# Performance work log

Measured on AMD Instinct MI355X. Metric: run time of the kernel, lower is better.

The kernel has to match this reference:

```python
import jax, jax.numpy as jnp
import numpy as np

IN_F, OUT_F = 2048, 2048
IQ, OQ = IN_F // 4, OUT_F // 4
B, S = 4, 4096


def _xavier(key, shape):
    fan_out, fan_in = shape
    limit = float(np.sqrt(6.0 / (fan_in + fan_out)))
    return jax.random.uniform(key, shape, jnp.float32, -limit, limit)


def setup_inputs() -> dict:
    key = jax.random.key(0)
    kx, kr, ki, kj, kk = jax.random.split(key, 5)
    return {
        "x": jax.random.normal(kx, (B, S, IN_F), dtype=jnp.float32),
        "wr": _xavier(kr, (OQ, IQ)),
        "wi": _xavier(ki, (OQ, IQ)),
        "wj": _xavier(kj, (OQ, IQ)),
        "wk": _xavier(kk, (OQ, IQ)),
        "bias": jnp.zeros((OUT_F,), dtype=jnp.float32),
    }


def reference(x, wr, wi, wj, wk, bias):
    b, s, _ = x.shape
    iq = wr.shape[1]
    oq = wr.shape[0]
    # strided quaternion component extraction: x[..., c::4] -> (B*S, iq)
    xq = x.reshape(b * s, iq, 4)  # last-dim interleaved layout
    xr, xi, xj, xk = xq[..., 0], xq[..., 1], xq[..., 2], xq[..., 3]
    # small GEMMs against W^T (W is (oq, iq)); only the products actually used
    Ar = xr @ wr.T
    Br = xi @ wr.T
    Cr = xj @ wr.T
    Dr = xk @ wr.T
    Ai = xr @ wi.T
    Bi = xi @ wi.T
    Aj = xr @ wj.T
    Cj = xj @ wj.T
    Ak = xr @ wk.T
    Dk = xk @ wk.T
    # combine exactly as in the original module
    or_ = Ar - Bi - Cj - Dk
    oi_ = Br + Ai + Dk - Cj
    oj_ = Cr - Dk + Aj + Bi
    ok_ = Dr + Cj - Bi + Ak
    # interleaved scatter: out[:, c::4] = o<c>
    out = jnp.stack([or_, oi_, oj_, ok_], axis=-1).reshape(b, s, 4 * oq)
    return out + bias[None, None, :]
```

## Files before the change

kernel.cpp:

```cpp
#include <hip/hip_runtime.h>


typedef unsigned short u16;
typedef __bf16 bf16x8 __attribute__((ext_vector_type(8)));
typedef float f32x16 __attribute__((ext_vector_type(16)));

#define QM 16384
#define QN 2048
#define QK 2048

__device__ __forceinline__ u16 f2bf(float f) {
    union { float f; unsigned u; } v;
    v.f = f;
    unsigned r = v.u + 0x7FFFu + ((v.u >> 16) & 1u);
    return (u16)(r >> 16);
}

__device__ __forceinline__ void async_copy16(const u16* g, u16* l) {
    __builtin_amdgcn_global_load_lds(
        (const __attribute__((address_space(1))) void*)g,
        (__attribute__((address_space(3))) void*)l,
        16, 0, 0);
}

__global__ void prep_kernel(const float* __restrict__ x, u16* __restrict__ xb,
                            const float* __restrict__ wr, const float* __restrict__ wi,
                            const float* __restrict__ wj, const float* __restrict__ wk,
                            u16* __restrict__ wb) {
    const int b = blockIdx.x;
    if (b < 4096) {
        const int n4 = (QM * QK) / 4;
        for (int i = b * blockDim.x + threadIdx.x; i < n4; i += 4096 * blockDim.x) {
            float4 v = reinterpret_cast<const float4*>(x)[i];
            ushort4 o;
            o.x = f2bf(v.x); o.y = f2bf(v.y); o.z = f2bf(v.z); o.w = f2bf(v.w);
            reinterpret_cast<ushort4*>(xb)[i] = o;
        }
    } else {
        int i = (b - 4096) * blockDim.x + threadIdx.x;
        int n = i >> 9;
        int p = i & 511;
        int q = n >> 2, co = n & 3;
        int base = (q << 9) + p;
        float r  = wr[base], ii = wi[base], jj = wj[base], kk = wk[base];
        float e0, e1, e2, e3;
        if      (co == 0) { e0 = r;  e1 = -ii; e2 = -jj; e3 = -kk; }
        else if (co == 1) { e0 = ii; e1 = r;   e2 = -jj; e3 = kk;  }
        else if (co == 2) { e0 = jj; e1 = ii;  e2 = r;   e3 = -kk; }
        else              { e0 = kk; e1 = -ii; e2 = jj;  e3 = r;   }
        ushort4 o;
        o.x = f2bf(e0); o.y = f2bf(e1); o.z = f2bf(e2); o.w = f2bf(e3);
        reinterpret_cast<ushort4*>(wb)[(n << 9) + p] = o;
    }
}

__global__ __launch_bounds__(512, 2) void qgemm_kernel(const u16* __restrict__ A,
                                                       const u16* __restrict__ B,
                                                       const float* __restrict__ bias,
                                                       float* __restrict__ C) {
    __shared__ __align__(16) u16 L[81920];

    const int bid = blockIdx.x;
    const int swz = (bid & 7) * 64 + (bid >> 3);
    const int bm = swz >> 3;
    const int bn = swz & 7;

    const int tid = threadIdx.x;
    const int wid = tid >> 6, lane = tid & 63;
    const int wm = wid >> 2, wn = wid & 3;
    const int lr = lane & 31;
    const int hi = lane >> 5;
    
    const u16* Asrc = A + (size_t)bm * 256 * QK;
    const u16* Bsrc = B + (size_t)bn * 256 * QK;

    const int rA  = tid >> 3;
    const int clA = ((tid & 7) ^ (rA & 7)) << 3;
    const size_t soff = (size_t)rA * QK + clA;

    f32x16 acc[4][2];
#pragma unroll
    for (int i = 0; i < 4; ++i)
#pragma unroll
        for (int j = 0; j < 2; ++j)
            acc[i][j] = (f32x16){0.f};

    auto stage = [&](const u16* src, int lbase, int k0) {
#pragma unroll
        for (int o = 0; o < 2; ++o)
            async_copy16(src + (size_t)(o * 64) * QK + k0 + soff,
                         &L[lbase + o * 4096 + wid * 512]);
    };

    auto rdA = [&](const u16* LA, int mt, int s) -> bf16x8 {
        const int r = wm * 128 + mt * 32 + lr;
        const int c = ((s * 2 + hi) ^ (r & 7)) << 3;
        return *(const bf16x8*)&LA[r * 64 + c];
    };
    auto rdB = [&](const u16* LB, int nt, int s) -> bf16x8 {
        const int r = wn * 64 + nt * 32 + lr;
        const int c = ((s * 2 + hi) ^ (r & 7)) << 3;
        return *(const bf16x8*)&LB[r * 64 + c];
    };

    auto doTile = [&](const int ab, const int bt, const int bt2, const int t)
        __attribute__((always_inline)) {
        const u16* LA = &L[ab * 16384];
        const u16* LB = &L[32768 + bt * 16384];
        const int tw1 = (t + 1) & 31, tw2 = (t + 2) & 31;
        const int oA = (ab ^ 1) * 16384;
        const int oB = 32768 + bt2 * 16384;

#pragma unroll
        for (int s = 0; s < 4; ++s) {
            bf16x8 bv[2], av[4];
#pragma unroll
            for (int nt = 0; nt < 2; ++nt) bv[nt] = rdB(LB, nt, s);
#pragma unroll
            for (int mt = 0; mt < 4; ++mt) av[mt] = rdA(LA, mt, s);
            if      (s == 0) stage(Asrc,            oA,        tw1 * 64);
            else if (s == 1) stage(Asrc + 128 * QK, oA + 8192, tw1 * 64);
            else if (s == 2) stage(Bsrc,            oB,        tw2 * 64);
            else             stage(Bsrc + 128 * QK, oB + 8192, tw2 * 64);
#pragma unroll
            for (int mt = 0; mt < 4; ++mt)
#pragma unroll
                for (int nt = 0; nt < 2; ++nt)
                    acc[mt][nt] = __builtin_amdgcn_mfma_f32_32x32x16_bf16(
                        av[mt], bv[nt], acc[mt][nt], 0, 0, 0);
        }

        asm volatile("s_waitcnt lgkmcnt(0) vmcnt(4)" ::: "memory");
        __builtin_amdgcn_s_barrier();
    };

    stage(Asrc,            0,             0);
    stage(Asrc + 128 * QK, 8192,          0);
    stage(Bsrc,            32768,             0);
    stage(Bsrc + 128 * QK, 32768 + 8192,      0);
    stage(Bsrc,            32768 + 16384,        64);
    stage(Bsrc + 128 * QK, 32768 + 16384 + 8192, 64);
    asm volatile("s_waitcnt vmcnt(4)" ::: "memory");
    __builtin_amdgcn_s_barrier();

    for (int t = 0; t < 30; t += 6) {
        doTile(0, 0, 2, t);
        doTile(1, 1, 0, t + 1);
        doTile(0, 2, 1, t + 2);
        doTile(1, 0, 2, t + 3);
        doTile(0, 1, 0, t + 4);
        doTile(1, 2, 1, t + 5);
    }
    doTile(0, 0, 2, 30);
    doTile(1, 1, 0, 31);

    const int colbase = bn * 256 + wn * 64;
    const int rowbase = bm * 256 + wm * 128;
    float bsv[2];
#pragma unroll
    for (int nt = 0; nt < 2; ++nt) bsv[nt] = bias[colbase + nt * 32 + lr];
    float* Cb = C + (size_t)rowbase * QN + colbase;
#pragma unroll
    for (int mt = 0; mt < 4; ++mt)
#pragma unroll
        for (int nt = 0; nt < 2; ++nt)
#pragma unroll
            for (int e = 0; e < 16; ++e) {
                const int ro = mt * 32 + (e & 3) + 8 * (e >> 2) + 4 * hi;
                Cb[(size_t)ro * QN + nt * 32 + lr] = acc[mt][nt][e] + bsv[nt];
            }
}

extern "C" void kernel_launch(void* const* d_in, const int* in_sizes, int n_in,
                              void* d_out, int out_size, void* d_ws, size_t ws_size,
                              hipStream_t stream) {
    const float* x    = (const float*)d_in[0];
    const float* wr   = (const float*)d_in[1];
    const float* wi   = (const float*)d_in[2];
    const float* wj   = (const float*)d_in[3];
    const float* wk   = (const float*)d_in[4];
    const float* bias = (const float*)d_in[5];
    float* out = (float*)d_out;

    u16* xb = (u16*)d_ws;
    u16* wb = (u16*)((char*)d_ws + (size_t)QM * QK * 2);

    prep_kernel<<<8192, 256, 0, stream>>>(x, xb, wr, wi, wj, wk, wb);
    qgemm_kernel<<<512, 512, 0, stream>>>(xb, wb, bias, out);
}
```

Measured before the change: 170.1 us.

## Switch LDS to k-chunk-major layout and software-pipeline LDS reads ahead of MFMAs

```diff
diff --git a/kernel.cpp b/kernel.cpp
--- a/kernel.cpp
+++ b/kernel.cpp
@@ -70,13 +70,12 @@
     const int wm = wid >> 2, wn = wid & 3;
     const int lr = lane & 31;
     const int hi = lane >> 5;
-    
+
     const u16* Asrc = A + (size_t)bm * 256 * QK;
     const u16* Bsrc = B + (size_t)bn * 256 * QK;
 
-    const int rA  = tid >> 3;
-    const int clA = ((tid & 7) ^ (rA & 7)) << 3;
-    const size_t soff = (size_t)rA * QK + clA;
+    const int srow = tid & 255;
+    const int scol0 = tid >> 8;
 
     f32x16 acc[4][2];
 #pragma unroll
@@ -85,74 +84,113 @@
         for (int j = 0; j < 2; ++j)
             acc[i][j] = (f32x16){0.f};
 
-    auto stage = [&](const u16* src, int lbase, int k0) {
-#pragma unroll
-        for (int o = 0; o < 2; ++o)
-            async_copy16(src + (size_t)(o * 64) * QK + k0 + soff,
-                         &L[lbase + o * 4096 + wid * 512]);
+    auto stage = [&](const u16* src, int lbase, int k0, int h) {
+#pragma unroll
+        for (int o = 0; o < 2; ++o) {
+            const int c = h * 4 + o * 2 + scol0;
+            async_copy16(src + (size_t)srow * QK + k0 + c * 8,
+                         &L[lbase + h * 8192 + o * 4096 + wid * 512]);
+        }
     };
 
     auto rdA = [&](const u16* LA, int mt, int s) -> bf16x8 {
         const int r = wm * 128 + mt * 32 + lr;
-        const int c = ((s * 2 + hi) ^ (r & 7)) << 3;
-        return *(const bf16x8*)&LA[r * 64 + c];
+        const int c = s * 2 + hi;
+        return *(const bf16x8*)&LA[c * 2048 + r * 8];
     };
     auto rdB = [&](const u16* LB, int nt, int s) -> bf16x8 {
         const int r = wn * 64 + nt * 32 + lr;
-        const int c = ((s * 2 + hi) ^ (r & 7)) << 3;
-        return *(const bf16x8*)&LB[r * 64 + c];
-    };
-
-    auto doTile = [&](const int ab, const int bt, const int bt2, const int t)
-        __attribute__((always_inline)) {
-        const u16* LA = &L[ab * 16384];
-        const u16* LB = &L[32768 + bt * 16384];
+        const int c = s * 2 + hi;
+        return *(const bf16x8*)&LB[c * 2048 + r * 8];
+    };
+
+    bf16x8 a0[4], b0[2];
+
+    auto doTile = [&](const int ab, const int bt, const int bt2,
+                      const int abn, const int btn, const int t,
+                      const bool preRead) __attribute__((always_inline)) {
+        const u16* LA  = &L[ab * 16384];
+        const u16* LB  = &L[32768 + bt * 16384];
+        const u16* LAn = &L[abn * 16384];
+        const u16* LBn = &L[32768 + btn * 16384];
         const int tw1 = (t + 1) & 31, tw2 = (t + 2) & 31;
-        const int oA = (ab ^ 1) * 16384;
+        const int oA = abn * 16384;
         const int oB = 32768 + bt2 * 16384;
 
-#pragma unroll
-        for (int s = 0; s < 4; ++s) {
-            bf16x8 bv[2], av[4];
-#pragma unroll
-            for (int nt = 0; nt < 2; ++nt) bv[nt] = rdB(LB, nt, s);
-#pragma unroll
-            for (int mt = 0; mt < 4; ++mt) av[mt] = rdA(LA, mt, s);
-            if      (s == 0) stage(Asrc,            oA,        tw1 * 64);
-            else if (s == 1) stage(Asrc + 128 * QK, oA + 8192, tw1 * 64);
-            else if (s == 2) stage(Bsrc,            oB,        tw2 * 64);
-            else             stage(Bsrc + 128 * QK, oB + 8192, tw2 * 64);
-#pragma unroll
-            for (int mt = 0; mt < 4; ++mt)
-#pragma unroll
-                for (int nt = 0; nt < 2; ++nt)
-                    acc[mt][nt] = __builtin_amdgcn_mfma_f32_32x32x16_bf16(
-                        av[mt], bv[nt], acc[mt][nt], 0, 0, 0);
-        }
-
+        bf16x8 a1[4], b1[2], a2[4], b2[2], a3[4], b3[2];
+
+        stage(Asrc, oA, tw1 * 64, 0);
+#pragma unroll
+        for (int nt = 0; nt < 2; ++nt) b1[nt] = rdB(LB, nt, 1);
+#pragma unroll
+        for (int mt = 0; mt < 4; ++mt) a1[mt] = rdA(LA, mt, 1);
+#pragma unroll
+        for (int mt = 0; mt < 4; ++mt)
+#pragma unroll
+            for (int nt = 0; nt < 2; ++nt)
+                acc[mt][nt] = __builtin_amdgcn_mfma_f32_32x32x16_bf16(a0[mt], b0[nt], acc[mt][nt], 0, 0, 0);
+
+        stage(Asrc, oA, tw1 * 64, 1);
+#pragma unroll
+        for (int nt = 0; nt < 2; ++nt) b2[nt] = rdB(LB, nt, 2);
+#pragma unroll
+        for (int mt = 0; mt < 4; ++mt) a2[mt] = rdA(LA, mt, 2);
+#pragma unroll
+        for (int mt = 0; mt < 4; ++mt)
+#pragma unroll
+            for (int nt = 0; nt < 2; ++nt)
+                acc[mt][nt] = __builtin_amdgcn_mfma_f32_32x32x16_bf16(a1[mt], b1[nt], acc[mt][nt], 0, 0, 0);
+
+        stage(Bsrc, oB, tw2 * 64, 0);
+#pragma unroll
+        for (int nt = 0; nt < 2; ++nt) b3[nt] = rdB(LB, nt, 3);
+#pragma unroll
+        for (int mt = 0; mt < 4; ++mt) a3[mt] = rdA(LA, mt, 3);
+#pragma unroll
+        for (int mt = 0; mt < 4; ++mt)
+#pragma unroll
+            for (int nt = 0; nt < 2; ++nt)
+                acc[mt][nt] = __builtin_amdgcn_mfma_f32_32x32x16_bf16(a2[mt], b2[nt], acc[mt][nt], 0, 0, 0);
+
+        stage(Bsrc, oB, tw2 * 64, 1);
         asm volatile("s_waitcnt lgkmcnt(0) vmcnt(4)" ::: "memory");
         __builtin_amdgcn_s_barrier();
-    };
-
-    stage(Asrc,            0,             0);
-    stage(Asrc + 128 * QK, 8192,          0);
-    stage(Bsrc,            32768,             0);
-    stage(Bsrc + 128 * QK, 32768 + 8192,      0);
-    stage(Bsrc,            32768 + 16384,        64);
-    stage(Bsrc + 128 * QK, 32768 + 16384 + 8192, 64);
+        if (preRead) {
+#pragma unroll
+            for (int nt = 0; nt < 2; ++nt) b0[nt] = rdB(LBn, nt, 0);
+#pragma unroll
+            for (int mt = 0; mt < 4; ++mt) a0[mt] = rdA(LAn, mt, 0);
+        }
+#pragma unroll
+        for (int mt = 0; mt < 4; ++mt)
+#pragma unroll
+            for (int nt = 0; nt < 2; ++nt)
+                acc[mt][nt] = __builtin_amdgcn_mfma_f32_32x32x16_bf16(a3[mt], b3[nt], acc[mt][nt], 0, 0, 0);
+    };
+
+    stage(Asrc, 0,     0, 0);
+    stage(Asrc, 0,     0, 1);
+    stage(Bsrc, 32768, 0, 0);
+    stage(Bsrc, 32768, 0, 1);
+    stage(Bsrc, 32768 + 16384, 64, 0);
+    stage(Bsrc, 32768 + 16384, 64, 1);
     asm volatile("s_waitcnt vmcnt(4)" ::: "memory");
     __builtin_amdgcn_s_barrier();
+#pragma unroll
+    for (int nt = 0; nt < 2; ++nt) b0[nt] = rdB(&L[32768], nt, 0);
+#pragma unroll
+    for (int mt = 0; mt < 4; ++mt) a0[mt] = rdA(&L[0], mt, 0);
 
     for (int t = 0; t < 30; t += 6) {
-        doTile(0, 0, 2, t);
-        doTile(1, 1, 0, t + 1);
-        doTile(0, 2, 1, t + 2);
-        doTile(1, 0, 2, t + 3);
-        doTile(0, 1, 0, t + 4);
-        doTile(1, 2, 1, t + 5);
+        doTile(0, 0, 2, 1, 1, t,     true);
+        doTile(1, 1, 0, 0, 2, t + 1, true);
+        doTile(0, 2, 1, 1, 0, t + 2, true);
+        doTile(1, 0, 2, 0, 1, t + 3, true);
+        doTile(0, 1, 0, 1, 2, t + 4, true);
+        doTile(1, 2, 1, 0, 0, t + 5, true);
     }
-    doTile(0, 0, 2, 30);
-    doTile(1, 1, 0, 31);
+    doTile(0, 0, 2, 1, 1, 30, true);
+    doTile(1, 1, 0, 0, 2, 31, false);
 
     const int colbase = bn * 256 + wn * 64;
     const int rowbase = bm * 256 + wm * 128;
```

After: 240.3 us. 1.41x slower.
